# Kernel optimization log

Measured on AMD Instinct MI355X. Metric: run time of the kernel, lower is better.

## Reference

```python
import jax, jax.numpy as jnp
import numpy as np

B, S, L = 64, 512, 768


def setup_inputs() -> dict:
    key = jax.random.key(0)
    k1, k2 = jax.random.split(key)
    x = jax.random.normal(k1, (B, S, L), dtype=jnp.float32)
    # matches torch uniform_(-0.1, 0.1) init for the probe matrix b
    b = jax.random.uniform(k2, (L, L), minval=-0.1, maxval=0.1, dtype=jnp.float32)
    return {"x": x, "b": b}


def reference(x, b):
    # Original: z[b,i,j,h] = x_i - x_j; h = einsum('gh,bijh', b, z); dist = sum_g h^2
    # Identity: ||b @ (x_i - x_j)||^2 = ||p_i||^2 + ||p_j||^2 - 2 p_i . p_j,  p = x @ b^T
    p = jnp.einsum('gh,bsh->bsg', b, x)          # [B, S, L] projected points
    sq = jnp.sum(p * p, axis=-1)                 # [B, S]  squared norms
    gram = jnp.einsum('bsg,btg->bst', p, p)      # [B, S, S] inner products
    return sq[:, :, None] + sq[:, None, :] - 2.0 * gram  # [B, S, S]
```

## Files before the change

kernel.cpp:

```cpp
#include <hip/hip_runtime.h>
#include <hip/hip_bf16.h>


using bf16x8 = __attribute__((ext_vector_type(8))) __bf16;
using f32x4  = __attribute__((ext_vector_type(4))) float;
using fl4    = __attribute__((ext_vector_type(4))) float;
using u16x4  = __attribute__((ext_vector_type(4))) unsigned short;

#define NB 64
#define NS 512
#define NL 768

__device__ __forceinline__ unsigned short f2bf(float f) {
  unsigned u = __builtin_bit_cast(unsigned, f);
  u += 0x7FFFu + ((u >> 16) & 1u);
  return (unsigned short)(u >> 16);
}

__device__ __forceinline__ void gload_lds16(const void* g, void* l) {
  __builtin_amdgcn_global_load_lds(
      (const __attribute__((address_space(1))) void*)g,
      (__attribute__((address_space(3))) void*)l, 16, 0, 0);
}

#define MEMFENCE asm volatile("" ::: "memory")

__global__ __launch_bounds__(256) void k_cvt_b(const float* __restrict__ b,
                                               unsigned short* __restrict__ bb) {
  const long t = (long)blockIdx.x * 256 + threadIdx.x;
  fl4 v = *(const fl4*)(b + t * 4);
  u16x4 o;
#pragma unroll
  for (int j = 0; j < 4; ++j) o[j] = f2bf(v[j]);
  *(u16x4*)(bb + t * 4) = o;
}

__global__ __launch_bounds__(256) void k_cvt_x(const float* __restrict__ x,
                                               unsigned short* __restrict__ xb) {
  const long n4 = (long)NB * NS * NL / 4;
  const long stride = (long)gridDim.x * 256;
  for (long i = (long)blockIdx.x * 256 + threadIdx.x; i < n4; i += stride) {
    fl4 v = *(const fl4*)(x + i * 4);
    u16x4 o;
#pragma unroll
    for (int j = 0; j < 4; ++j) o[j] = f2bf(v[j]);
    *(u16x4*)(xb + i * 4) = o;
  }
}

__global__ __launch_bounds__(256, 2) void k_projb(
    const unsigned short* __restrict__ xb,
    const unsigned short* __restrict__ bb,
    unsigned short* __restrict__ p) {
  __shared__ __align__(16) unsigned short smA[3][128 * 32];
  __shared__ __align__(16) unsigned short smB[3][256 * 32];
  const int tid = threadIdx.x;
  const int w = tid >> 6, l = tid & 63;
  const int wg = ((blockIdx.x & 7) * 96) + (blockIdx.x >> 3);
  const int nt = wg % 3, mt = wg / 3;
  const long m0 = (long)mt * 128, n0 = (long)nt * 256;
  const int wr = (w >> 1) * 64, wc = (w & 1) * 128;

  const int srow = tid >> 2;
  const int scol = ((tid & 3) ^ ((srow >> 1) & 3)) * 8;
  const unsigned short* gA = xb + (m0 + srow) * (long)NL + scol;
  const unsigned short* gB = bb + (n0 + srow) * (long)NL + scol;

  const int qh = l >> 4, lr = l & 15;
  const int swz = ((qh ^ ((lr >> 1) & 3)) << 4);
  const int aoff = (wr + lr) * 64 + swz;
  const int boff = (wc + lr) * 64 + swz;

  f32x4 acc[4][8] = {};

#define STAGEP(k0, buf)                                                      \
  {                                                                          \
    char* da_ = (char*)&smA[buf][0] + w * 1024;                              \
    char* db_ = (char*)&smB[buf][0] + w * 1024;                              \
    gload_lds16(gA + (k0), da_);                                             \
    gload_lds16(gA + (k0) + 64 * NL, da_ + 4096);                            \
    gload_lds16(gB + (k0), db_);                                             \
    gload_lds16(gB + (k0) + 64 * NL, db_ + 4096);                            \
    gload_lds16(gB + (k0) + 128 * NL, db_ + 8192);                           \
    gload_lds16(gB + (k0) + 192 * NL, db_ + 12288);                          \
  }
#define COMPUTEP(buf)                                                        \
  {                                                                          \
    const char* A_ = (const char*)&smA[buf][0];                              \
    const char* B_ = (const char*)&smB[buf][0];                              \
    bf16x8 fa[4], fb[8];                                                     \
    _Pragma("unroll")                                                        \
    for (int m = 0; m < 4; ++m)                                              \
      fa[m] = *(const bf16x8*)(A_ + aoff + m * 1024);                        \
    _Pragma("unroll")                                                        \
    for (int n = 0; n < 8; ++n)                                              \
      fb[n] = *(const bf16x8*)(B_ + boff + n * 1024);                        \
    _Pragma("unroll")                                                        \
    for (int m = 0; m < 4; ++m)                                              \
      _Pragma("unroll")                                                      \
      for (int n = 0; n < 8; ++n)                                            \
        acc[m][n] = __builtin_amdgcn_mfma_f32_16x16x32_bf16(fa[m], fb[n],    \
                                                            acc[m][n], 0, 0, 0); \
  }

  STAGEP(0, 0)
  STAGEP(32, 1)
  int cur = 0, nxt2 = 2;
#pragma unroll 1
  for (int kt = 0; kt < 23; ++kt) {
    asm volatile("s_waitcnt vmcnt(6)" ::: "memory");
    __builtin_amdgcn_s_barrier();
    MEMFENCE;
    if (kt < 22) STAGEP((kt + 2) * 32, nxt2)
    COMPUTEP(cur)
    cur = (cur == 2) ? 0 : cur + 1;
    nxt2 = (nxt2 == 2) ? 0 : nxt2 + 1;
  }
  asm volatile("s_waitcnt vmcnt(0)" ::: "memory");
  __builtin_amdgcn_s_barrier();
  MEMFENCE;
  COMPUTEP(cur)
#undef STAGEP
#undef COMPUTEP

#pragma unroll
  for (int m = 0; m < 4; ++m) {
    const long rbase = m0 + wr + m * 16 + qh * 4;
#pragma unroll
    for (int n = 0; n < 8; ++n) {
      const long col = n0 + wc + n * 16 + lr;
#pragma unroll
      for (int r = 0; r < 4; ++r)
        p[(rbase + r) * NL + col] = f2bf(acc[m][n][r]);
    }
  }
}

__global__ __launch_bounds__(256) void k_sq(const unsigned short* __restrict__ p,
                                            float* __restrict__ sq) {
  const int row = blockIdx.x * 4 + (threadIdx.x >> 6);
  const int l = threadIdx.x & 63;
  const unsigned short* pr = p + (long)row * NL;
  float s = 0.f;
#pragma unroll
  for (int c = 0; c < 3; ++c) {
    u16x4 v = *(const u16x4*)(pr + (c * 64 + l) * 4);
#pragma unroll
    for (int j = 0; j < 4; ++j) {
      float f = __builtin_bit_cast(float, ((unsigned)v[j]) << 16);
      s += f * f;
    }
  }
#pragma unroll
  for (int d = 32; d >= 1; d >>= 1) s += __shfl_xor(s, d, 64);
  if (l == 0) sq[row] = s;
}

__global__ __launch_bounds__(256, 2) void k_gram(
    const unsigned short* __restrict__ p,
    const float* __restrict__ sq,
    float* __restrict__ out) {
  __shared__ __align__(16) unsigned short smA[3][128 * 32];
  __shared__ __align__(16) unsigned short smB[3][256 * 32];
  const int tid = threadIdx.x;
  const int w = tid >> 6, l = tid & 63;
  const int wg = ((blockIdx.x & 7) * 64) + (blockIdx.x >> 3);
  const int batch = wg >> 3, tile = wg & 7;
  const int mt = tile >> 1, nt = tile & 1;
  const unsigned short* pb = p + (long)batch * NS * NL;
  const long m0 = (long)mt * 128, n0 = (long)nt * 256;
  const int wr = (w >> 1) * 64, wc = (w & 1) * 128;

  const int srow = tid >> 2;
  const int scol = ((tid & 3) ^ ((srow >> 1) & 3)) * 8;
  const unsigned short* gA = pb + (m0 + srow) * (long)NL + scol;
  const unsigned short* gB = pb + (n0 + srow) * (long)NL + scol;

  const int qh = l >> 4, lr = l & 15;
  const int swz = ((qh ^ ((lr >> 1) & 3)) << 4);
  const int aoff = (wr + lr) * 64 + swz;
  const int boff = (wc + lr) * 64 + swz;

  f32x4 acc[4][8] = {};

#define STAGEG(k0, buf)                                                      \
  {                                                                          \
    char* da_ = (char*)&smA[buf][0] + w * 1024;                              \
    char* db_ = (char*)&smB[buf][0] + w * 1024;                              \
    gload_lds16(gA + (k0), da_);                                             \
    gload_lds16(gA + (k0) + 64 * NL, da_ + 4096);                            \
    gload_lds16(gB + (k0), db_);                                             \
    gload_lds16(gB + (k0) + 64 * NL, db_ + 4096);                            \
    gload_lds16(gB + (k0) + 128 * NL, db_ + 8192);                           \
    gload_lds16(gB + (k0) + 192 * NL, db_ + 12288);                          \
  }
#define COMPUTEG(buf)                                                        \
  {                                                                          \
    const char* A_ = (const char*)&smA[buf][0];                              \
    const char* B_ = (const char*)&smB[buf][0];                              \
    bf16x8 fa[4], fb[8];                                                     \
    _Pragma("unroll")                                                        \
    for (int m = 0; m < 4; ++m)                                              \
      fa[m] = *(const bf16x8*)(A_ + aoff + m * 1024);                        \
    _Pragma("unroll")                                                        \
    for (int n = 0; n < 8; ++n)                                              \
      fb[n] = *(const bf16x8*)(B_ + boff + n * 1024);                        \
    _Pragma("unroll")                                                        \
    for (int m = 0; m < 4; ++m)                                              \
      _Pragma("unroll")                                                      \
      for (int n = 0; n < 8; ++n)                                            \
        acc[m][n] = __builtin_amdgcn_mfma_f32_16x16x32_bf16(fa[m], fb[n],    \
                                                            acc[m][n], 0, 0, 0); \
  }

  STAGEG(0, 0)
  STAGEG(32, 1)
  int cur = 0, nxt2 = 2;
#pragma unroll 1
  for (int kt = 0; kt < 23; ++kt) {
    asm volatile("s_waitcnt vmcnt(6)" ::: "memory");
    __builtin_amdgcn_s_barrier();
    MEMFENCE;
    if (kt < 22) STAGEG((kt + 2) * 32, nxt2)
    COMPUTEG(cur)
    cur = (cur == 2) ? 0 : cur + 1;
    nxt2 = (nxt2 == 2) ? 0 : nxt2 + 1;
  }
  asm volatile("s_waitcnt vmcnt(0)" ::: "memory");
  __builtin_amdgcn_s_barrier();
  MEMFENCE;
  COMPUTEG(cur)
#undef STAGEG
#undef COMPUTEG

  const float* sqb = sq + batch * NS;
  float* outb = out + (long)batch * NS * NS;
  float sqc[8];
#pragma unroll
  for (int n = 0; n < 8; ++n) sqc[n] = sqb[n0 + wc + n * 16 + lr];
#pragma unroll
  for (int m = 0; m < 4; ++m) {
#pragma unroll
    for (int r = 0; r < 4; ++r) {
      const long row = m0 + wr + m * 16 + qh * 4 + r;
      const float sr = sqb[row];
#pragma unroll
      for (int n = 0; n < 8; ++n) {
        const long col = n0 + wc + n * 16 + lr;
        outb[row * NS + col] = sr + sqc[n] - 2.0f * acc[m][n][r];
      }
    }
  }
}

extern "C" void kernel_launch(void* const* d_in, const int* in_sizes, int n_in,
                              void* d_out, int out_size, void* d_ws, size_t ws_size,
                              hipStream_t stream) {
  (void)in_sizes; (void)n_in; (void)out_size; (void)ws_size;
  const float* x = (const float*)d_in[0];
  const float* b = (const float*)d_in[1];
  float* out = (float*)d_out;
  char* ws = (char*)d_ws;
  unsigned short* bb = (unsigned short*)ws;
  float* sq          = (float*)(ws + 1179648);
  unsigned short* p  = (unsigned short*)(ws + 1310720);
  unsigned short* xb = (unsigned short*)(ws + 51642368);

  k_cvt_b<<<576, 256, 0, stream>>>(b, bb);
  k_cvt_x<<<2048, 256, 0, stream>>>(x, xb);
  k_projb<<<768, 256, 0, stream>>>(xb, bb, p);
  k_sq   <<<8192, 256, 0, stream>>>(p, sq);
  k_gram <<<512, 256, 0, stream>>>(p, sq, out);
}
```

Before: 133.6 us.

## Fuse squared-norm into projection epilogue, shrink gram tiles, double-buffer projection

```diff
diff --git a/kernel.cpp b/kernel.cpp
--- a/kernel.cpp
+++ b/kernel.cpp
@@ -36,7 +36,9 @@
 }
 
 __global__ __launch_bounds__(256) void k_cvt_x(const float* __restrict__ x,
-                                               unsigned short* __restrict__ xb) {
+                                               unsigned short* __restrict__ xb,
+                                               float* __restrict__ sq) {
+  if (blockIdx.x < 128) sq[blockIdx.x * 256 + threadIdx.x] = 0.f;
   const long n4 = (long)NB * NS * NL / 4;
   const long stride = (long)gridDim.x * 256;
   for (long i = (long)blockIdx.x * 256 + threadIdx.x; i < n4; i += stride) {
@@ -48,12 +50,13 @@
   }
 }
 
-__global__ __launch_bounds__(256, 2) void k_projb(
+__global__ __launch_bounds__(256, 3) void k_projb(
     const unsigned short* __restrict__ xb,
     const unsigned short* __restrict__ bb,
-    unsigned short* __restrict__ p) {
-  __shared__ __align__(16) unsigned short smA[3][128 * 32];
-  __shared__ __align__(16) unsigned short smB[3][256 * 32];
+    unsigned short* __restrict__ p,
+    float* __restrict__ sq) {
+  __shared__ __align__(16) unsigned short smA[2][128 * 32];
+  __shared__ __align__(16) unsigned short smB[2][256 * 32];
   const int tid = threadIdx.x;
   const int w = tid >> 6, l = tid & 63;
   const int wg = ((blockIdx.x & 7) * 96) + (blockIdx.x >> 3);
@@ -104,22 +107,21 @@
   }
 
   STAGEP(0, 0)
-  STAGEP(32, 1)
-  int cur = 0, nxt2 = 2;
-#pragma unroll 1
-  for (int kt = 0; kt < 23; ++kt) {
-    asm volatile("s_waitcnt vmcnt(6)" ::: "memory");
-    __builtin_amdgcn_s_barrier();
-    MEMFENCE;
-    if (kt < 22) STAGEP((kt + 2) * 32, nxt2)
-    COMPUTEP(cur)
-    cur = (cur == 2) ? 0 : cur + 1;
-    nxt2 = (nxt2 == 2) ? 0 : nxt2 + 1;
-  }
   asm volatile("s_waitcnt vmcnt(0)" ::: "memory");
   __builtin_amdgcn_s_barrier();
   MEMFENCE;
-  COMPUTEP(cur)
+  int cur = 0;
+#pragma unroll 1
+  for (int kt = 0; kt < 24; ++kt) {
+    if (kt < 23) STAGEP((kt + 1) * 32, cur ^ 1)
+    COMPUTEP(cur)
+    if (kt < 23) {
+      asm volatile("s_waitcnt vmcnt(0)" ::: "memory");
+      __builtin_amdgcn_s_barrier();
+      MEMFENCE;
+      cur ^= 1;
+    }
+  }
 #undef STAGEP
 #undef COMPUTEP
 
@@ -127,49 +129,38 @@
   for (int m = 0; m < 4; ++m) {
     const long rbase = m0 + wr + m * 16 + qh * 4;
 #pragma unroll
-    for (int n = 0; n < 8; ++n) {
-      const long col = n0 + wc + n * 16 + lr;
-#pragma unroll
-      for (int r = 0; r < 4; ++r)
-        p[(rbase + r) * NL + col] = f2bf(acc[m][n][r]);
+    for (int r = 0; r < 4; ++r) {
+      const long row = rbase + r;
+      float s = 0.f;
+#pragma unroll
+      for (int n = 0; n < 8; ++n) {
+        const unsigned short us = f2bf(acc[m][n][r]);
+        p[row * NL + (n0 + wc + n * 16 + lr)] = us;
+        const float f = __builtin_bit_cast(float, ((unsigned)us) << 16);
+        s += f * f;
+      }
+      s += __shfl_xor(s, 1, 64);
+      s += __shfl_xor(s, 2, 64);
+      s += __shfl_xor(s, 4, 64);
+      s += __shfl_xor(s, 8, 64);
+      if (lr == 0) atomicAdd(sq + row, s);
     }
   }
 }
 
-__global__ __launch_bounds__(256) void k_sq(const unsigned short* __restrict__ p,
-                                            float* __restrict__ sq) {
-  const int row = blockIdx.x * 4 + (threadIdx.x >> 6);
-  const int l = threadIdx.x & 63;
-  const unsigned short* pr = p + (long)row * NL;
-  float s = 0.f;
-#pragma unroll
-  for (int c = 0; c < 3; ++c) {
-    u16x4 v = *(const u16x4*)(pr + (c * 64 + l) * 4);
-#pragma unroll
-    for (int j = 0; j < 4; ++j) {
-      float f = __builtin_bit_cast(float, ((unsigned)v[j]) << 16);
-      s += f * f;
-    }
-  }
-#pragma unroll
-  for (int d = 32; d >= 1; d >>= 1) s += __shfl_xor(s, d, 64);
-  if (l == 0) sq[row] = s;
-}
-
-__global__ __launch_bounds__(256, 2) void k_gram(
-    const unsigned short* __restrict__ p,
-    const float* __restrict__ sq,
-    float* __restrict__ out) {
+__global__ __launch_bounds__(256) void k_gram(const unsigned short* __restrict__ p,
+                                              const float* __restrict__ sq,
+                                              float* __restrict__ out) {
   __shared__ __align__(16) unsigned short smA[3][128 * 32];
-  __shared__ __align__(16) unsigned short smB[3][256 * 32];
+  __shared__ __align__(16) unsigned short smB[3][128 * 32];
   const int tid = threadIdx.x;
   const int w = tid >> 6, l = tid & 63;
-  const int wg = ((blockIdx.x & 7) * 64) + (blockIdx.x >> 3);
-  const int batch = wg >> 3, tile = wg & 7;
-  const int mt = tile >> 1, nt = tile & 1;
+  const int wg = ((blockIdx.x & 7) * 128) + (blockIdx.x >> 3);
+  const int batch = wg >> 4, tile = wg & 15;
+  const int mt = tile >> 2, nt = tile & 3;
   const unsigned short* pb = p + (long)batch * NS * NL;
-  const long m0 = (long)mt * 128, n0 = (long)nt * 256;
-  const int wr = (w >> 1) * 64, wc = (w & 1) * 128;
+  const long m0 = (long)mt * 128, n0 = (long)nt * 128;
+  const int wr = (w >> 1) * 64, wc = (w & 1) * 64;
 
   const int srow = tid >> 2;
   const int scol = ((tid & 3) ^ ((srow >> 1) & 3)) * 8;
@@ -177,13 +168,12 @@
   const unsigned short* gB = pb + (n0 + srow) * (long)NL + scol;
 
   const int qh = l >> 4, lr = l & 15;
-  const int swz = ((qh ^ ((lr >> 1) & 3)) << 4);
-  const int aoff = (wr + lr) * 64 + swz;
-  const int boff = (wc + lr) * 64 + swz;
-
-  f32x4 acc[4][8] = {};
-
-#define STAGEG(k0, buf)                                                      \
+  const int aoff = (wr + lr) * 64 + ((qh ^ ((lr >> 1) & 3)) << 4);
+  const int boff = (wc + lr) * 64 + ((qh ^ ((lr >> 1) & 3)) << 4);
+
+  f32x4 acc[4][4] = {};
+
+#define STAGE2(k0, buf)                                                      \
   {                                                                          \
     char* da_ = (char*)&smA[buf][0] + w * 1024;                              \
     char* db_ = (char*)&smB[buf][0] + w * 1024;                              \
@@ -191,53 +181,51 @@
     gload_lds16(gA + (k0) + 64 * NL, da_ + 4096);                            \
     gload_lds16(gB + (k0), db_);                                             \
     gload_lds16(gB + (k0) + 64 * NL, db_ + 4096);                            \
-    gload_lds16(gB + (k0) + 128 * NL, db_ + 8192);                           \
-    gload_lds16(gB + (k0) + 192 * NL, db_ + 12288);                          \
-  }
-#define COMPUTEG(buf)                                                        \
+  }
+#define COMPUTE2(buf)                                                        \
   {                                                                          \
     const char* A_ = (const char*)&smA[buf][0];                              \
     const char* B_ = (const char*)&smB[buf][0];                              \
-    bf16x8 fa[4], fb[8];                                                     \
+    bf16x8 fa[4], fb[4];                                                     \
     _Pragma("unroll")                                                        \
     for (int m = 0; m < 4; ++m)                                              \
       fa[m] = *(const bf16x8*)(A_ + aoff + m * 1024);                        \
     _Pragma("unroll")                                                        \
-    for (int n = 0; n < 8; ++n)                                              \
+    for (int n = 0; n < 4; ++n)                                              \
       fb[n] = *(const bf16x8*)(B_ + boff + n * 1024);                        \
     _Pragma("unroll")                                                        \
     for (int m = 0; m < 4; ++m)                                              \
       _Pragma("unroll")                                                      \
-      for (int n = 0; n < 8; ++n)                                            \
+      for (int n = 0; n < 4; ++n)                                            \
         acc[m][n] = __builtin_amdgcn_mfma_f32_16x16x32_bf16(fa[m], fb[n],    \
                                                             acc[m][n], 0, 0, 0); \
   }
 
-  STAGEG(0, 0)
-  STAGEG(32, 1)
+  STAGE2(0, 0)
+  STAGE2(32, 1)
   int cur = 0, nxt2 = 2;
 #pragma unroll 1
   for (int kt = 0; kt < 23; ++kt) {
-    asm volatile("s_waitcnt vmcnt(6)" ::: "memory");
+    asm volatile("s_waitcnt vmcnt(4)" ::: "memory");
     __builtin_amdgcn_s_barrier();
     MEMFENCE;
-    if (kt < 22) STAGEG((kt + 2) * 32, nxt2)
-    COMPUTEG(cur)
+    if (kt < 22) STAGE2((kt + 2) * 32, nxt2)
+    COMPUTE2(cur)
     cur = (cur == 2) ? 0 : cur + 1;
     nxt2 = (nxt2 == 2) ? 0 : nxt2 + 1;
   }
   asm volatile("s_waitcnt vmcnt(0)" ::: "memory");
   __builtin_amdgcn_s_barrier();
   MEMFENCE;
-  COMPUTEG(cur)
-#undef STAGEG
-#undef COMPUTEG
+  COMPUTE2(cur)
+#undef STAGE2
+#undef COMPUTE2
 
   const float* sqb = sq + batch * NS;
   float* outb = out + (long)batch * NS * NS;
-  float sqc[8];
-#pragma unroll
-  for (int n = 0; n < 8; ++n) sqc[n] = sqb[n0 + wc + n * 16 + lr];
+  float sqc[4];
+#pragma unroll
+  for (int n = 0; n < 4; ++n) sqc[n] = sqb[n0 + wc + n * 16 + lr];
 #pragma unroll
   for (int m = 0; m < 4; ++m) {
 #pragma unroll
@@ -245,7 +233,7 @@
       const long row = m0 + wr + m * 16 + qh * 4 + r;
       const float sr = sqb[row];
 #pragma unroll
-      for (int n = 0; n < 8; ++n) {
+      for (int n = 0; n < 4; ++n) {
         const long col = n0 + wc + n * 16 + lr;
         outb[row * NS + col] = sr + sqc[n] - 2.0f * acc[m][n][r];
       }
@@ -267,8 +255,7 @@
   unsigned short* xb = (unsigned short*)(ws + 51642368);
 
   k_cvt_b<<<576, 256, 0, stream>>>(b, bb);
-  k_cvt_x<<<2048, 256, 0, stream>>>(x, xb);
-  k_projb<<<768, 256, 0, stream>>>(xb, bb, p);
-  k_sq   <<<8192, 256, 0, stream>>>(p, sq);
-  k_gram <<<512, 256, 0, stream>>>(p, sq, out);
-}
+  k_cvt_x<<<2048, 256, 0, stream>>>(x, xb, sq);
+  k_projb<<<768, 256, 0, stream>>>(xb, bb, p, sq);
+  k_gram <<<1024, 256, 0, stream>>>(p, sq, out);
+}
```

After: 137.4 us. +2.9%, slower.
